# Optimization experiments

Hardware: AMD Instinct MI355X
Metric: run time of the kernel (lower is better)

## Reference

```python
import jax, jax.numpy as jnp
import numpy as np


def setup_inputs() -> dict:
    key = jax.random.key(0)
    ks = jax.random.split(key, 4)
    B, T, D, H = 128, 512, 256, 512
    scale = 1.0 / np.sqrt(D)
    return {
        "x": jax.random.normal(ks[0], (B, T, D), dtype=jnp.float32),
        "h0": jnp.zeros((B, H), dtype=jnp.float32),
        "kernelr": jax.random.normal(ks[1], (D, H), dtype=jnp.float32) * scale,
        "kernelz": jax.random.normal(ks[2], (D, H), dtype=jnp.float32) * scale,
        "kernelh": jax.random.normal(ks[3], (D, H), dtype=jnp.float32) * scale,
        "memoryr": jnp.ones((H,), dtype=jnp.float32),
        "memoryz": jnp.ones((H,), dtype=jnp.float32),
        "br": jnp.zeros((H,), dtype=jnp.float32),
        "bz": jnp.zeros((H,), dtype=jnp.float32),
    }


def reference(x, h0, kernelr, kernelz, kernelh, memoryr, memoryz, br, bz):
    # Precompute all input projections as one batched GEMM over (B*T, D).
    # xr/xz/xh: [T, B, H]
    xr = jnp.einsum("btd,dh->tbh", x, kernelr) + br
    xz = jnp.einsum("btd,dh->tbh", x, kernelz) + bz
    xh = jnp.einsum("btd,dh->tbh", x, kernelh)

    def step(h, inp):
        pr, pz, ph = inp
        r = jnp.tanh(pr + h * memoryr) + 1.0
        z = jax.nn.sigmoid(pz + h * memoryz)
        out = z * h + (1.0 - z) * jnp.tanh(ph + r * h)
        return out, out

    _, outs = jax.lax.scan(step, h0, (xr, xz, xh))  # outs: [T, B, H]
    return jnp.transpose(outs, (1, 0, 2))  # [B, T, H]
```

## Files before the change

kernel.cpp:

```cpp
#include <hip/hip_runtime.h>

typedef _Float16 f16;
typedef _Float16 f16x8 __attribute__((ext_vector_type(8)));
typedef _Float16 f16x4 __attribute__((ext_vector_type(4)));
typedef float f32x4 __attribute__((ext_vector_type(4)));

__device__ __forceinline__ float rcpf(float x) { return __builtin_amdgcn_rcpf(x); }

__global__ void __launch_bounds__(256) cvt_w(const float* __restrict__ Wr,
                                             const float* __restrict__ Wz,
                                             const float* __restrict__ Wh,
                                             f16* __restrict__ out) {
  int o = blockIdx.x * 256 + threadIdx.x;
  int rl = o & 15, ni = (o >> 4) & 3, kq = (o >> 6) & 3, kt = (o >> 8) & 7;
  int wnt = o >> 11;
  int w = wnt % 3, nt = wnt / 3;
  int n = nt * 64 + ni * 16 + rl;
  int k0 = kt * 32 + kq * 8;
  const float* W = (w == 0) ? Wr : ((w == 1) ? Wz : Wh);
  f16x8 v;
#pragma unroll
  for (int e = 0; e < 8; ++e) v[e] = (f16)W[(size_t)(k0 + e) * 512 + n];
  *(f16x8*)(out + (size_t)o * 8) = v;
}

__global__ void __launch_bounds__(256) cvt_x(const float* __restrict__ in,
                                             f16* __restrict__ out) {
  int o = blockIdx.x * 256 + threadIdx.x;
  int rl = o & 15, kq = (o >> 4) & 3, kt = (o >> 6) & 7, m16 = o >> 9;
  const float* src = in + (size_t)(m16 * 16 + rl) * 256 + kt * 32 + kq * 8;
  f16x8 v;
#pragma unroll
  for (int e = 0; e < 8; ++e) v[e] = (f16)src[e];
  *(f16x8*)(out + (size_t)o * 8) = v;
}

__global__ void __launch_bounds__(256, 3) brc_fused(
    const f16* __restrict__ Af, const f16* __restrict__ Bf,
    const float* __restrict__ h0, const float* __restrict__ mr,
    const float* __restrict__ mz, const float* __restrict__ br,
    const float* __restrict__ bz, float* __restrict__ out) {
  __shared__ __align__(16) f16 Pl[2][12288];
  const int tid = threadIdx.x;
  const int wid = tid >> 6, lane = tid & 63;
  const int bid = blockIdx.x;
  const int lid = (bid & 7) * 128 + (bid >> 3);
  const int b = lid >> 3, hs = lid & 7;

  const int w3 = wid < 3 ? wid : 0;
  const char* Ap = (const char*)Af + lane * 16;
  const char* Bp = (const char*)Bf + (lane >> 4) * 1024 + (lane & 15) * 16 +
                   (size_t)(hs * 3 + w3) * 32768;
  const int col = lane & 15, rbase = (lane >> 4) * 4;

  float h = 0.f, mrc = 0.f, mzc = 0.f, br2 = 0.f, nbz = 0.f;
  if (wid == 3) {
    int hg = hs * 64 + lane;
    h = h0[(size_t)b * 512 + hg];
    mrc = 2.0f * mr[hg]; mzc = -mz[hg];
    br2 = 2.0f * br[hg]; nbz = -bz[hg];
  }

#define LOADF(AA, BB, q, kt)                                                  \
  do {                                                                        \
    _Pragma("unroll") for (int mi = 0; mi < 4; ++mi)                          \
      AA[mi] = *(const f16x8*)(Ap +                                           \
                (size_t)((b * 32 + (q) * 4 + mi) * 8 + (kt)) * 1024);         \
    _Pragma("unroll") for (int ni = 0; ni < 4; ++ni)                          \
      BB[ni] = *(const f16x8*)(Bp + (size_t)(kt) * 4096 + ni * 256);          \
  } while (0)

#define MFMA16(AA, BB)                                                        \
  do {                                                                        \
    _Pragma("unroll") for (int mi = 0; mi < 4; ++mi)                          \
      _Pragma("unroll") for (int ni = 0; ni < 4; ++ni)                        \
        acc[mi][ni] = __builtin_amdgcn_mfma_f32_16x16x32_f16(                 \
            AA[mi], BB[ni], acc[mi][ni], 0, 0, 0);                            \
  } while (0)

  auto gemm_phase = [&](int q) {
    f16* Pb = Pl[q & 1];
    f32x4 acc[4][4] = {};
    f16x8 aE[4], bE[4], aO[4], bO[4];
    LOADF(aE, bE, q, 0);
#pragma unroll
    for (int kt = 0; kt < 8; kt += 2) {
      LOADF(aO, bO, q, kt + 1);
      __builtin_amdgcn_s_setprio(1);
      MFMA16(aE, bE);
      __builtin_amdgcn_s_setprio(0);
      if (kt + 2 < 8) LOADF(aE, bE, q, kt + 2);
      __builtin_amdgcn_s_setprio(1);
      MFMA16(aO, bO);
      __builtin_amdgcn_s_setprio(0);
    }
#pragma unroll
    for (int mi = 0; mi < 4; ++mi) {
      int tl = mi * 16 + rbase;
#pragma unroll
      for (int ni = 0; ni < 4; ++ni) {
        int hl = ni * 16 + col;
        f16x4 v;
#pragma unroll
        for (int r = 0; r < 4; ++r) v[r] = (f16)acc[mi][ni][r];
        *(f16x4*)&Pb[w3 * 4096 + (tl >> 3) * 512 + hl * 8 + (tl & 7)] = v;
      }
    }
  };

  if (wid < 3) gemm_phase(0);

  for (int p = 0; p < 8; ++p) {
    __syncthreads();
    if (wid < 3) {
      if (p + 1 < 8) gemm_phase(p + 1);
    } else {
      const f16* Pb = Pl[p & 1];
      float* opm = out + ((size_t)b * 512 + p * 64) * 512 + hs * 64 + lane;
#pragma unroll
      for (int tg = 0; tg < 8; ++tg) {
        f16x8 R  = *(const f16x8*)&Pb[tg * 512 + lane * 8];
        f16x8 Z  = *(const f16x8*)&Pb[4096 + tg * 512 + lane * 8];
        f16x8 Hh = *(const f16x8*)&Pb[8192 + tg * 512 + lane * 8];
#pragma unroll
        for (int j = 0; j < 8; ++j) {
          float prs = fmaf((float)R[j], 2.0f, br2);
          float pzs = fmaf((float)Z[j], -1.0f, nbz);
          float ph2 = (float)Hh[j] * 2.0f;
          float er = __expf(fmaf(h, mrc, prs));
          float rr = fmaf(-2.0f, rcpf(er + 1.0f), 2.0f);
          float ez = __expf(fmaf(h, mzc, pzs));
          float zz = rcpf(1.0f + ez);
          float ec = __expf(fmaf(rr, h + h, ph2));
          float cd = fmaf(-2.0f, rcpf(ec + 1.0f), 1.0f);
          h = fmaf(zz, h - cd, cd);
          __builtin_nontemporal_store(h, opm + (size_t)(tg * 8 + j) * 512);
        }
      }
    }
  }
#undef LOADF
#undef MFMA16
}

extern "C" void kernel_launch(void* const* d_in, const int* in_sizes, int n_in,
                              void* d_out, int out_size, void* d_ws, size_t ws_size,
                              hipStream_t stream) {
  const float* x  = (const float*)d_in[0];
  const float* h0 = (const float*)d_in[1];
  const float* kr = (const float*)d_in[2];
  const float* kz = (const float*)d_in[3];
  const float* kh = (const float*)d_in[4];
  const float* mr = (const float*)d_in[5];
  const float* mz = (const float*)d_in[6];
  const float* br = (const float*)d_in[7];
  const float* bz = (const float*)d_in[8];
  float* out = (float*)d_out;

  f16* Bf = (f16*)d_ws;
  f16* Xf = Bf + 393216;

  cvt_w<<<192, 256, 0, stream>>>(kr, kz, kh, Bf);
  cvt_x<<<8192, 256, 0, stream>>>(x, Xf);
  brc_fused<<<1024, 256, 0, stream>>>(Xf, Bf, h0, mr, mz, br, bz, out);
}
```

Before: 134.1 us.

## Stage A tiles into LDS via global_load_lds, merge conversion kernels, use exp2

The three GEMM waves now cooperatively copy each phase's shared X tile into LDS with direct global-to-LDS loads, instead of each wave loading the same A fragments from global memory. The two conversion kernels are merged into a single launch, and the recurrence uses exp2 with log2(e) folded into the constants, removing a multiply per exponential. This adds LDS use and an extra barrier per phase, and lowers the occupancy hint from 3 to 2 blocks per CU.

```diff
diff --git a/kernel.cpp b/kernel.cpp
--- a/kernel.cpp
+++ b/kernel.cpp
@@ -6,41 +6,52 @@
 typedef float f32x4 __attribute__((ext_vector_type(4)));
 
 __device__ __forceinline__ float rcpf(float x) { return __builtin_amdgcn_rcpf(x); }
+__device__ __forceinline__ float exp2f_(float x) { return __builtin_amdgcn_exp2f(x); }
 
-__global__ void __launch_bounds__(256) cvt_w(const float* __restrict__ Wr,
-                                             const float* __restrict__ Wz,
-                                             const float* __restrict__ Wh,
-                                             f16* __restrict__ out) {
-  int o = blockIdx.x * 256 + threadIdx.x;
-  int rl = o & 15, ni = (o >> 4) & 3, kq = (o >> 6) & 3, kt = (o >> 8) & 7;
-  int wnt = o >> 11;
-  int w = wnt % 3, nt = wnt / 3;
-  int n = nt * 64 + ni * 16 + rl;
-  int k0 = kt * 32 + kq * 8;
-  const float* W = (w == 0) ? Wr : ((w == 1) ? Wz : Wh);
-  f16x8 v;
-#pragma unroll
-  for (int e = 0; e < 8; ++e) v[e] = (f16)W[(size_t)(k0 + e) * 512 + n];
-  *(f16x8*)(out + (size_t)o * 8) = v;
+__device__ __forceinline__ void gload_lds16(const void* g, void* l) {
+  __builtin_amdgcn_global_load_lds(
+      (const __attribute__((address_space(1))) void*)g,
+      (__attribute__((address_space(3))) void*)l, 16, 0, 0);
 }
 
-__global__ void __launch_bounds__(256) cvt_x(const float* __restrict__ in,
-                                             f16* __restrict__ out) {
-  int o = blockIdx.x * 256 + threadIdx.x;
-  int rl = o & 15, kq = (o >> 4) & 3, kt = (o >> 6) & 7, m16 = o >> 9;
-  const float* src = in + (size_t)(m16 * 16 + rl) * 256 + kt * 32 + kq * 8;
-  f16x8 v;
+#define LOG2E 1.4426950408889634f
+
+__global__ void __launch_bounds__(256) cvt_all(const float* __restrict__ x,
+                                               const float* __restrict__ Wr,
+                                               const float* __restrict__ Wz,
+                                               const float* __restrict__ Wh,
+                                               f16* __restrict__ Bf,
+                                               f16* __restrict__ Xf) {
+  if (blockIdx.x < 192) {
+    int o = blockIdx.x * 256 + threadIdx.x;
+    int rl = o & 15, ni = (o >> 4) & 3, kq = (o >> 6) & 3, kt = (o >> 8) & 7;
+    int wnt = o >> 11;
+    int w = wnt % 3, nt = wnt / 3;
+    int n = nt * 64 + ni * 16 + rl;
+    int k0 = kt * 32 + kq * 8;
+    const float* W = (w == 0) ? Wr : ((w == 1) ? Wz : Wh);
+    f16x8 v;
 #pragma unroll
-  for (int e = 0; e < 8; ++e) v[e] = (f16)src[e];
-  *(f16x8*)(out + (size_t)o * 8) = v;
+    for (int e = 0; e < 8; ++e) v[e] = (f16)W[(size_t)(k0 + e) * 512 + n];
+    *(f16x8*)(Bf + (size_t)o * 8) = v;
+  } else {
+    int o = (blockIdx.x - 192) * 256 + threadIdx.x;
+    int rl = o & 15, kq = (o >> 4) & 3, kt = (o >> 6) & 7, m16 = o >> 9;
+    const float* src = x + (size_t)(m16 * 16 + rl) * 256 + kt * 32 + kq * 8;
+    f16x8 v;
+#pragma unroll
+    for (int e = 0; e < 8; ++e) v[e] = (f16)src[e];
+    *(f16x8*)(Xf + (size_t)o * 8) = v;
+  }
 }
 
-__global__ void __launch_bounds__(256, 3) brc_fused(
+__global__ void __launch_bounds__(256, 2) brc_fused(
     const f16* __restrict__ Af, const f16* __restrict__ Bf,
     const float* __restrict__ h0, const float* __restrict__ mr,
     const float* __restrict__ mz, const float* __restrict__ br,
     const float* __restrict__ bz, float* __restrict__ out) {
   __shared__ __align__(16) f16 Pl[2][12288];
+  __shared__ __align__(16) f16 Al[16384];
   const int tid = threadIdx.x;
   const int wid = tid >> 6, lane = tid & 63;
   const int bid = blockIdx.x;
@@ -48,26 +59,36 @@
   const int b = lid >> 3, hs = lid & 7;
 
   const int w3 = wid < 3 ? wid : 0;
-  const char* Ap = (const char*)Af + lane * 16;
   const char* Bp = (const char*)Bf + (lane >> 4) * 1024 + (lane & 15) * 16 +
                    (size_t)(hs * 3 + w3) * 32768;
   const int col = lane & 15, rbase = (lane >> 4) * 4;
 
-  float h = 0.f, mrc = 0.f, mzc = 0.f, br2 = 0.f, nbz = 0.f;
+  float h = 0.f, mrcL = 0.f, mzL = 0.f, brL = 0.f, bzL = 0.f;
   if (wid == 3) {
     int hg = hs * 64 + lane;
     h = h0[(size_t)b * 512 + hg];
-    mrc = 2.0f * mr[hg]; mzc = -mz[hg];
-    br2 = 2.0f * br[hg]; nbz = -bz[hg];
+    mrcL = 2.0f * LOG2E * mr[hg]; mzL = -LOG2E * mz[hg];
+    brL = 2.0f * LOG2E * br[hg]; bzL = -LOG2E * bz[hg];
   }
 
-#define LOADF(AA, BB, q, kt)                                                  \
+#define STAGEA(q)                                                             \
+  do {                                                                        \
+    const char* gsrc = (const char*)Af + ((size_t)(b * 32 + (q) * 4) * 8) * 1024; \
+    for (int j = wid; j < 32; j += 3)                                         \
+      gload_lds16(gsrc + (size_t)j * 1024 + lane * 16, (char*)Al + j * 1024); \
+  } while (0)
+
+#define LOADB(BB, kt)                                                         \
+  do {                                                                        \
+    _Pragma("unroll") for (int ni = 0; ni < 4; ++ni)                          \
+      BB[ni] = *(const f16x8*)(Bp + (size_t)(kt) * 4096 + ni * 256);          \
+  } while (0)
+
+#define LOADA(AA, kt)                                                         \
   do {                                                                        \
     _Pragma("unroll") for (int mi = 0; mi < 4; ++mi)                          \
-      AA[mi] = *(const f16x8*)(Ap +                                           \
-                (size_t)((b * 32 + (q) * 4 + mi) * 8 + (kt)) * 1024);         \
-    _Pragma("unroll") for (int ni = 0; ni < 4; ++ni)                          \
-      BB[ni] = *(const f16x8*)(Bp + (size_t)(kt) * 4096 + ni * 256);          \
+      AA[mi] = *(const f16x8*)((const char*)Al + (mi * 8 + (kt)) * 1024 +     \
+                               lane * 16);                                    \
   } while (0)
 
 #define MFMA16(AA, BB)                                                        \
@@ -81,17 +102,21 @@
   auto gemm_phase = [&](int q) {
     f16* Pb = Pl[q & 1];
     f32x4 acc[4][4] = {};
-    f16x8 aE[4], bE[4], aO[4], bO[4];
-    LOADF(aE, bE, q, 0);
+    f16x8 a[4], bE[4], bO[4];
+    LOADB(bE, 0);
 #pragma unroll
     for (int kt = 0; kt < 8; kt += 2) {
-      LOADF(aO, bO, q, kt + 1);
+      if (kt + 1 < 8) LOADB(bO, kt + 1);
+      __builtin_amdgcn_sched_barrier(0);
+      LOADA(a, kt);
       __builtin_amdgcn_s_setprio(1);
-      MFMA16(aE, bE);
+      MFMA16(a, bE);
       __builtin_amdgcn_s_setprio(0);
-      if (kt + 2 < 8) LOADF(aE, bE, q, kt + 2);
+      if (kt + 2 < 8) LOADB(bE, kt + 2);
+      __builtin_amdgcn_sched_barrier(0);
+      LOADA(a, kt + 1);
       __builtin_amdgcn_s_setprio(1);
-      MFMA16(aO, bO);
+      MFMA16(a, bO);
       __builtin_amdgcn_s_setprio(0);
     }
 #pragma unroll
@@ -108,9 +133,13 @@
     }
   };
 
+  if (wid < 3) STAGEA(0);
+  __syncthreads();
   if (wid < 3) gemm_phase(0);
 
   for (int p = 0; p < 8; ++p) {
+    __syncthreads();
+    if (wid < 3 && p + 1 < 8) STAGEA(p + 1);
     __syncthreads();
     if (wid < 3) {
       if (p + 1 < 8) gemm_phase(p + 1);
@@ -124,14 +153,15 @@
         f16x8 Hh = *(const f16x8*)&Pb[8192 + tg * 512 + lane * 8];
 #pragma unroll
         for (int j = 0; j < 8; ++j) {
-          float prs = fmaf((float)R[j], 2.0f, br2);
-          float pzs = fmaf((float)Z[j], -1.0f, nbz);
-          float ph2 = (float)Hh[j] * 2.0f;
-          float er = __expf(fmaf(h, mrc, prs));
+          float prs = fmaf((float)R[j], 2.0f * LOG2E, brL);
+          float pzs = fmaf((float)Z[j], -LOG2E, bzL);
+          float phL = (float)Hh[j] * (2.0f * LOG2E);
+          float er = exp2f_(fmaf(h, mrcL, prs));
           float rr = fmaf(-2.0f, rcpf(er + 1.0f), 2.0f);
-          float ez = __expf(fmaf(h, mzc, pzs));
+          float ez = exp2f_(fmaf(h, mzL, pzs));
           float zz = rcpf(1.0f + ez);
-          float ec = __expf(fmaf(rr, h + h, ph2));
+          float h2L = h * (2.0f * LOG2E);
+          float ec = exp2f_(fmaf(rr, h2L, phL));
           float cd = fmaf(-2.0f, rcpf(ec + 1.0f), 1.0f);
           h = fmaf(zz, h - cd, cd);
           __builtin_nontemporal_store(h, opm + (size_t)(tg * 8 + j) * 512);
@@ -139,7 +169,9 @@
       }
     }
   }
-#undef LOADF
+#undef STAGEA
+#undef LOADB
+#undef LOADA
 #undef MFMA16
 }
 
@@ -160,7 +192,6 @@
   f16* Bf = (f16*)d_ws;
   f16* Xf = Bf + 393216;
 
-  cvt_w<<<192, 256, 0, stream>>>(kr, kz, kh, Bf);
-  cvt_x<<<8192, 256, 0, stream>>>(x, Xf);
+  cvt_all<<<8384, 256, 0, stream>>>(x, kr, kz, kh, Bf, Xf);
   brc_fused<<<1024, 256, 0, stream>>>(Xf, Bf, h0, mr, mz, br, bz, out);
 }
```

After: 110.2 us. 1.22x faster.
